# Optimization experiments

Measured on AMD Instinct MI355X. Metric: run time of the kernel, lower is better.

Reference implementation:

```python
import jax, jax.numpy as jnp
import numpy as np

ALPHA = 0.2

def setup_inputs() -> dict:
    key = jax.random.key(0)
    k1, k2, k3, k4, k5 = jax.random.split(key, 5)
    B, N, Fin, Fout = 4, 4096, 128, 128
    x = jax.random.normal(k1, (B, N, Fin), dtype=jnp.float32)
    adj = jax.random.randint(k2, (N, N), 0, 2, dtype=jnp.int32)
    W = jax.random.normal(k3, (Fin, Fout), dtype=jnp.float32) * (1.0 / np.sqrt(Fin))
    a_src = jax.random.normal(k4, (Fout, 1), dtype=jnp.float32) * (1.0 / np.sqrt(Fout))
    a_dst = jax.random.normal(k5, (Fout, 1), dtype=jnp.float32) * (1.0 / np.sqrt(Fout))
    return {"x": x, "adj": adj, "W": W, "a_src": a_src, "a_dst": a_dst}

def reference(x, adj, W, a_src, a_dst):
    # h: (B, N, Fout)
    h = jnp.einsum('bnf,fo->bno', x, W)
    e_src = h @ a_src              # (B, N, 1)
    e_dst = h @ a_dst              # (B, N, 1)
    # additive attention scores: (B, N, N)
    e = e_src + jnp.swapaxes(e_dst, 1, 2)
    e = jnp.where(e >= 0, e, ALPHA * e)  # leaky_relu
    mask = (adj == 0)[None, :, :]
    e = jnp.where(mask, -jnp.inf, e)
    attn = jax.nn.softmax(e, axis=-1)
    attn = jnp.where(jnp.isnan(attn), 0.0, attn)  # nan_to_num for all-masked rows
    out = jnp.einsum('bij,bjo->bio', attn, h)
    return (out, attn)
```

## Files before the change

kernel.cpp:

```cpp
#include <hip/hip_runtime.h>
#include <hip/hip_bf16.h>
#include <hip/hip_fp16.h>

#define B_ 4
#define N_ 4096
#define F_ 128
#define NEG (-1e30f)

typedef _Float16 f16;
typedef _Float16 half8 __attribute__((ext_vector_type(8)));
typedef _Float16 half4 __attribute__((ext_vector_type(4)));
typedef float f32x4 __attribute__((ext_vector_type(4)));

__global__ void k_wa(const float* __restrict__ W, const float* __restrict__ a_src,
                     const float* __restrict__ a_dst, float* __restrict__ Wa) {
    int f = threadIdx.x;
    float s0 = 0.f, s1 = 0.f;
    for (int o = 0; o < F_; ++o) {
        float w = W[f * F_ + o];
        s0 += w * a_src[o];
        s1 += w * a_dst[o];
    }
    Wa[f] = s0;
    Wa[F_ + f] = s1;
}

__global__ __launch_bounds__(256) void k_h(const float* __restrict__ x,
                                           const float* __restrict__ W,
                                           f16* __restrict__ hT) {
    __shared__ float xs[16][128];
    int t = threadIdx.x;
    long R0 = (long)blockIdx.x * 16;
    const float4* xg = (const float4*)(x + R0 * 128);
    float4* xsv = (float4*)&xs[0][0];
    xsv[t] = xg[t];
    xsv[t + 256] = xg[t + 256];
    __syncthreads();
    int c = t & 127;
    int rg = t >> 7;
    float acc[8] = {0, 0, 0, 0, 0, 0, 0, 0};
    for (int k = 0; k < 128; ++k) {
        float wv = W[k * 128 + c];
        #pragma unroll
        for (int q = 0; q < 8; ++q) acc[q] += xs[rg * 8 + q][k] * wv;
    }
    int b = (int)(R0 >> 12);
    int i = (int)(R0 & 4095);
    half8 hv;
    #pragma unroll
    for (int q = 0; q < 8; ++q) hv[q] = (f16)acc[q];
    *(half8*)(hT + ((long)(b * 128 + c) * 4096 + i + rg * 8)) = hv;
}

__global__ __launch_bounds__(256) void k_e(const float* __restrict__ x,
                                           const float* __restrict__ Wa,
                                           float* __restrict__ e_src,
                                           float* __restrict__ e_dst) {
    int t = threadIdx.x;
    int lane = t & 63;
    int w = t >> 6;
    long rg = (long)blockIdx.x * 4 + w;
    const float* xr = x + rg * 128;
    float x0 = xr[lane], x1 = xr[lane + 64];
    float s = x0 * Wa[lane] + x1 * Wa[lane + 64];
    float d = x0 * Wa[128 + lane] + x1 * Wa[192 + lane];
    #pragma unroll
    for (int off = 32; off; off >>= 1) {
        s += __shfl_xor(s, off, 64);
        d += __shfl_xor(d, off, 64);
    }
    if (lane == 0) { e_src[rg] = s; e_dst[rg] = d; }
}

__global__ __launch_bounds__(256) void k_attn(const int* __restrict__ adj,
                                              const float* __restrict__ e_src,
                                              const float* __restrict__ e_dst,
                                              float* __restrict__ attn) {
    int rg = blockIdx.x;
    int b = rg >> 12;
    int i = rg & 4095;
    int t = threadIdx.x;
    float es = e_src[rg];
    const int* arow = adj + (long)i * N_;
    const float* ed = e_dst + b * N_;
    float p[16];
    float m = NEG;
    #pragma unroll
    for (int c = 0; c < 16; ++c) {
        int j = t + 256 * c;
        int a = arow[j];
        float e = es + ed[j];
        e = (e >= 0.f) ? e : 0.2f * e;
        e = a ? e : NEG;
        p[c] = e;
        m = fmaxf(m, e);
    }
    #pragma unroll
    for (int off = 32; off; off >>= 1) m = fmaxf(m, __shfl_xor(m, off, 64));
    __shared__ float sred[8];
    int lane = t & 63, wid = t >> 6;
    if (lane == 0) sred[wid] = m;
    __syncthreads();
    m = fmaxf(fmaxf(sred[0], sred[1]), fmaxf(sred[2], sred[3]));
    float sum = 0.f;
    #pragma unroll
    for (int c = 0; c < 16; ++c) {
        float pv = __expf(p[c] - m);
        p[c] = pv;
        sum += pv;
    }
    #pragma unroll
    for (int off = 32; off; off >>= 1) sum += __shfl_xor(sum, off, 64);
    if (lane == 0) sred[4 + wid] = sum;
    __syncthreads();
    sum = sred[4] + sred[5] + sred[6] + sred[7];
    float inv = (m <= -1e29f) ? 0.f : 1.f / sum;
    float* orow = attn + (long)rg * N_;
    #pragma unroll
    for (int c = 0; c < 16; ++c) orow[t + 256 * c] = p[c] * inv;
}

__global__ __launch_bounds__(256) void k_out(const float* __restrict__ attn,
                                             const f16* __restrict__ hT,
                                             float* __restrict__ out) {
    __shared__ __align__(16) f16 Alds[32][40];
    __shared__ __align__(16) f16 Blds[128][40];
    int t = threadIdx.x;
    int bx = blockIdx.x;
    int b = bx >> 7;
    int i0 = (bx & 127) * 32;
    const float* Ab = attn + ((long)b * N_ + i0) * N_;
    const f16* Bb = hT + (long)b * 128 * 4096;

    int lane = t & 63, wid = t >> 6;
    int strip = (wid & 1) * 16;
    int cb = (wid >> 1) * 64;
    int r16 = lane & 15;
    int kq = (lane >> 4) * 8;

    f32x4 acc[4] = {{0,0,0,0}, {0,0,0,0}, {0,0,0,0}, {0,0,0,0}};

    int ar = t >> 3;
    int akc = (t & 7) * 4;
    int bc = t & 127;
    int bh = t >> 7;

    for (int kt = 0; kt < 128; ++kt) {
        int k0 = kt * 32;
        __syncthreads();
        float4 av = *(const float4*)(Ab + (long)ar * N_ + k0 + akc);
        half4 a4;
        a4[0] = (f16)av.x; a4[1] = (f16)av.y; a4[2] = (f16)av.z; a4[3] = (f16)av.w;
        *(half4*)&Alds[ar][akc] = a4;
        const f16* bsrc = Bb + (long)bc * 4096 + k0 + bh * 16;
        half8 b0 = *(const half8*)(bsrc);
        half8 b1 = *(const half8*)(bsrc + 8);
        *(half8*)&Blds[bc][bh * 16] = b0;
        *(half8*)&Blds[bc][bh * 16 + 8] = b1;
        __syncthreads();
        half8 af = *(const half8*)&Alds[strip + r16][kq];
        #pragma unroll
        for (int nt = 0; nt < 4; ++nt) {
            half8 bf = *(const half8*)&Blds[cb + nt * 16 + r16][kq];
            acc[nt] = __builtin_amdgcn_mfma_f32_16x16x32_f16(af, bf, acc[nt], 0, 0, 0);
        }
    }
    int rbase = i0 + strip + (lane >> 4) * 4;
    float* ob = out + (long)b * N_ * 128;
    #pragma unroll
    for (int nt = 0; nt < 4; ++nt) {
        int col = cb + nt * 16 + r16;
        #pragma unroll
        for (int reg = 0; reg < 4; ++reg) {
            ob[(long)(rbase + reg) * 128 + col] = acc[nt][reg];
        }
    }
}

extern "C" void kernel_launch(void* const* d_in, const int* in_sizes, int n_in,
                              void* d_out, int out_size, void* d_ws, size_t ws_size,
                              hipStream_t stream) {
    const float* x     = (const float*)d_in[0];
    const int*   adj   = (const int*)d_in[1];
    const float* W     = (const float*)d_in[2];
    const float* a_src = (const float*)d_in[3];
    const float* a_dst = (const float*)d_in[4];
    float* out  = (float*)d_out;
    float* attn = out + (long)B_ * N_ * F_;

    char* ws = (char*)d_ws;
    float* Wa    = (float*)(ws + 0);
    float* e_src = (float*)(ws + 1024);
    float* e_dst = (float*)(ws + 66560);
    f16*   hT    = (f16*)(ws + 132096);

    k_wa<<<dim3(1), dim3(128), 0, stream>>>(W, a_src, a_dst, Wa);
    k_h<<<dim3((B_ * N_) / 16), dim3(256), 0, stream>>>(x, W, hT);
    k_e<<<dim3((B_ * N_) / 4), dim3(256), 0, stream>>>(x, Wa, e_src, e_dst);
    k_attn<<<dim3(B_ * N_), dim3(256), 0, stream>>>(adj, e_src, e_dst, attn);
    k_out<<<dim3(B_ * (N_ / 32)), dim3(256), 0, stream>>>(attn, hT, out);
}
```

Measured before the change: 525.5 us.

## Load MFMA fragments directly from global with register double-buffering in k_out

```diff
diff --git a/kernel.cpp b/kernel.cpp
--- a/kernel.cpp
+++ b/kernel.cpp
@@ -9,7 +9,6 @@
 
 typedef _Float16 f16;
 typedef _Float16 half8 __attribute__((ext_vector_type(8)));
-typedef _Float16 half4 __attribute__((ext_vector_type(4)));
 typedef float f32x4 __attribute__((ext_vector_type(4)));
 
 __global__ void k_wa(const float* __restrict__ W, const float* __restrict__ a_src,
@@ -123,56 +122,84 @@
 __global__ __launch_bounds__(256) void k_out(const float* __restrict__ attn,
                                              const f16* __restrict__ hT,
                                              float* __restrict__ out) {
-    __shared__ __align__(16) f16 Alds[32][40];
-    __shared__ __align__(16) f16 Blds[128][40];
-    int t = threadIdx.x;
+    int t = threadIdx.x;
+    int lane = t & 63, wid = t >> 6;
     int bx = blockIdx.x;
     int b = bx >> 7;
     int i0 = (bx & 127) * 32;
-    const float* Ab = attn + ((long)b * N_ + i0) * N_;
-    const f16* Bb = hT + (long)b * 128 * 4096;
-
-    int lane = t & 63, wid = t >> 6;
+    int r16 = lane & 15;
+    int kq = (lane >> 4) * 8;
     int strip = (wid & 1) * 16;
     int cb = (wid >> 1) * 64;
-    int r16 = lane & 15;
-    int kq = (lane >> 4) * 8;
-
-    f32x4 acc[4] = {{0,0,0,0}, {0,0,0,0}, {0,0,0,0}, {0,0,0,0}};
-
-    int ar = t >> 3;
-    int akc = (t & 7) * 4;
-    int bc = t & 127;
-    int bh = t >> 7;
-
-    for (int kt = 0; kt < 128; ++kt) {
-        int k0 = kt * 32;
-        __syncthreads();
-        float4 av = *(const float4*)(Ab + (long)ar * N_ + k0 + akc);
-        half4 a4;
-        a4[0] = (f16)av.x; a4[1] = (f16)av.y; a4[2] = (f16)av.z; a4[3] = (f16)av.w;
-        *(half4*)&Alds[ar][akc] = a4;
-        const f16* bsrc = Bb + (long)bc * 4096 + k0 + bh * 16;
-        half8 b0 = *(const half8*)(bsrc);
-        half8 b1 = *(const half8*)(bsrc + 8);
-        *(half8*)&Blds[bc][bh * 16] = b0;
-        *(half8*)&Blds[bc][bh * 16 + 8] = b1;
-        __syncthreads();
-        half8 af = *(const half8*)&Alds[strip + r16][kq];
-        #pragma unroll
-        for (int nt = 0; nt < 4; ++nt) {
-            half8 bf = *(const half8*)&Blds[cb + nt * 16 + r16][kq];
-            acc[nt] = __builtin_amdgcn_mfma_f32_16x16x32_f16(af, bf, acc[nt], 0, 0, 0);
-        }
-    }
+
+    const float* Ap = attn + ((long)b * N_ + i0 + strip + r16) * N_ + kq;
+    const f16* Bp = hT + ((long)(b * F_ + cb + r16)) * (long)N_ + kq;
+
+    f32x4 acc[4] = {{0,0,0,0},{0,0,0,0},{0,0,0,0},{0,0,0,0}};
+
+    f32x4 cA[2][2], nA[2][2];
+    half8 cB[2][4], nB[2][4];
+
+    #pragma unroll
+    for (int s = 0; s < 2; ++s) {
+        cA[s][0] = *(const f32x4*)(Ap + s * 32);
+        cA[s][1] = *(const f32x4*)(Ap + s * 32 + 4);
+        #pragma unroll
+        for (int nt = 0; nt < 4; ++nt)
+            cB[s][nt] = *(const half8*)(Bp + (long)nt * (16 * N_) + s * 32);
+    }
+
+    for (int kt = 1; kt < 64; ++kt) {
+        int k0 = kt * 64;
+        #pragma unroll
+        for (int s = 0; s < 2; ++s) {
+            nA[s][0] = *(const f32x4*)(Ap + k0 + s * 32);
+            nA[s][1] = *(const f32x4*)(Ap + k0 + s * 32 + 4);
+            #pragma unroll
+            for (int nt = 0; nt < 4; ++nt)
+                nB[s][nt] = *(const half8*)(Bp + (long)nt * (16 * N_) + k0 + s * 32);
+        }
+        #pragma unroll
+        for (int s = 0; s < 2; ++s) {
+            half8 af;
+            #pragma unroll
+            for (int q = 0; q < 4; ++q) {
+                af[q] = (f16)cA[s][0][q];
+                af[q + 4] = (f16)cA[s][1][q];
+            }
+            #pragma unroll
+            for (int nt = 0; nt < 4; ++nt)
+                acc[nt] = __builtin_amdgcn_mfma_f32_16x16x32_f16(af, cB[s][nt], acc[nt], 0, 0, 0);
+        }
+        #pragma unroll
+        for (int s = 0; s < 2; ++s) {
+            cA[s][0] = nA[s][0];
+            cA[s][1] = nA[s][1];
+            #pragma unroll
+            for (int nt = 0; nt < 4; ++nt) cB[s][nt] = nB[s][nt];
+        }
+    }
+    #pragma unroll
+    for (int s = 0; s < 2; ++s) {
+        half8 af;
+        #pragma unroll
+        for (int q = 0; q < 4; ++q) {
+            af[q] = (f16)cA[s][0][q];
+            af[q + 4] = (f16)cA[s][1][q];
+        }
+        #pragma unroll
+        for (int nt = 0; nt < 4; ++nt)
+            acc[nt] = __builtin_amdgcn_mfma_f32_16x16x32_f16(af, cB[s][nt], acc[nt], 0, 0, 0);
+    }
+
     int rbase = i0 + strip + (lane >> 4) * 4;
-    float* ob = out + (long)b * N_ * 128;
+    float* ob = out + (long)b * N_ * F_;
     #pragma unroll
     for (int nt = 0; nt < 4; ++nt) {
         int col = cb + nt * 16 + r16;
         #pragma unroll
         for (int reg = 0; reg < 4; ++reg) {
-            ob[(long)(rbase + reg) * 128 + col] = acc[nt][reg];
+            ob[(long)(rbase + reg) * F_ + col] = acc[nt][reg];
         }
     }
 }
```

Measured after the change: 546.3 us. 1.04x slower.

## Fuse attention weight recomputation with attn@h matmul using precomputed row stats

Applied to the files above, without the earlier changes.

```diff
diff --git a/kernel.cpp b/kernel.cpp
--- a/kernel.cpp
+++ b/kernel.cpp
@@ -9,17 +9,20 @@
 
 typedef _Float16 f16;
 typedef _Float16 half8 __attribute__((ext_vector_type(8)));
-typedef _Float16 half4 __attribute__((ext_vector_type(4)));
 typedef float f32x4 __attribute__((ext_vector_type(4)));
 
 __global__ void k_wa(const float* __restrict__ W, const float* __restrict__ a_src,
                      const float* __restrict__ a_dst, float* __restrict__ Wa) {
     int f = threadIdx.x;
+    const float4* Wr = (const float4*)(W + f * F_);
+    const float4* As = (const float4*)a_src;
+    const float4* Ad = (const float4*)a_dst;
     float s0 = 0.f, s1 = 0.f;
-    for (int o = 0; o < F_; ++o) {
-        float w = W[f * F_ + o];
-        s0 += w * a_src[o];
-        s1 += w * a_dst[o];
+    #pragma unroll
+    for (int o = 0; o < 32; ++o) {
+        float4 w = Wr[o], s = As[o], d = Ad[o];
+        s0 += w.x * s.x + w.y * s.y + w.z * s.z + w.w * s.w;
+        s1 += w.x * d.x + w.y * d.y + w.z * d.z + w.w * d.w;
     }
     Wa[f] = s0;
     Wa[F_ + f] = s1;
@@ -39,6 +42,7 @@
     int c = t & 127;
     int rg = t >> 7;
     float acc[8] = {0, 0, 0, 0, 0, 0, 0, 0};
+    #pragma unroll 4
     for (int k = 0; k < 128; ++k) {
         float wv = W[k * 128 + c];
         #pragma unroll
@@ -72,17 +76,19 @@
     if (lane == 0) { e_src[rg] = s; e_dst[rg] = d; }
 }
 
-__global__ __launch_bounds__(256) void k_attn(const int* __restrict__ adj,
-                                              const float* __restrict__ e_src,
-                                              const float* __restrict__ e_dst,
-                                              float* __restrict__ attn) {
-    int rg = blockIdx.x;
-    int b = rg >> 12;
-    int i = rg & 4095;
+__global__ __launch_bounds__(256) void k_stats(const int* __restrict__ adj,
+                                               const float* __restrict__ e_src,
+                                               const float* __restrict__ e_dst,
+                                               float* __restrict__ stat_m,
+                                               float* __restrict__ stat_inv) {
+    int bx = blockIdx.x;
+    int b = bx & 3;
+    int i = bx >> 2;
+    long rg = (long)b * N_ + i;
     int t = threadIdx.x;
     float es = e_src[rg];
     const int* arow = adj + (long)i * N_;
-    const float* ed = e_dst + b * N_;
+    const float* ed = e_dst + (long)b * N_;
     float p[16];
     float m = NEG;
     #pragma unroll
@@ -104,76 +110,107 @@
     m = fmaxf(fmaxf(sred[0], sred[1]), fmaxf(sred[2], sred[3]));
     float sum = 0.f;
     #pragma unroll
-    for (int c = 0; c < 16; ++c) {
-        float pv = __expf(p[c] - m);
-        p[c] = pv;
-        sum += pv;
-    }
+    for (int c = 0; c < 16; ++c) sum += __expf(p[c] - m);
     #pragma unroll
     for (int off = 32; off; off >>= 1) sum += __shfl_xor(sum, off, 64);
     if (lane == 0) sred[4 + wid] = sum;
     __syncthreads();
-    sum = sred[4] + sred[5] + sred[6] + sred[7];
-    float inv = (m <= -1e29f) ? 0.f : 1.f / sum;
-    float* orow = attn + (long)rg * N_;
-    #pragma unroll
-    for (int c = 0; c < 16; ++c) orow[t + 256 * c] = p[c] * inv;
-}
-
-__global__ __launch_bounds__(256) void k_out(const float* __restrict__ attn,
-                                             const f16* __restrict__ hT,
-                                             float* __restrict__ out) {
-    __shared__ __align__(16) f16 Alds[32][40];
-    __shared__ __align__(16) f16 Blds[128][40];
-    int t = threadIdx.x;
+    if (t == 0) {
+        sum = sred[4] + sred[5] + sred[6] + sred[7];
+        float inv = (m <= -1e29f) ? 0.f : 1.f / sum;
+        stat_m[rg] = m;
+        stat_inv[rg] = inv;
+    }
+}
+
+__device__ __forceinline__ void tile_step(
+    const int* Aj, const float* Ed, const f16* Bp, float* Ao,
+    int j0, int jn, float es, float m, float inv, int q4,
+    int4& a0c, int4& a1c, float4& e0c, float4& e1c,
+    int4& a0n, int4& a1n, float4& e0n, float4& e1n,
+    f32x4& acc0, f32x4& acc1) {
+    a0n = *(const int4*)(Aj + jn);
+    a1n = *(const int4*)(Aj + jn + 4);
+    e0n = *(const float4*)(Ed + jn);
+    e1n = *(const float4*)(Ed + jn + 4);
+    half8 bf0 = *(const half8*)(Bp + j0);
+    half8 bf1 = *(const half8*)(Bp + j0 + 16 * N_);
+    int am[8] = {a0c.x, a0c.y, a0c.z, a0c.w, a1c.x, a1c.y, a1c.z, a1c.w};
+    float ev[8] = {e0c.x, e0c.y, e0c.z, e0c.w, e1c.x, e1c.y, e1c.z, e1c.w};
+    float pv[8];
+    #pragma unroll
+    for (int q = 0; q < 8; ++q) {
+        float e = es + ev[q];
+        e = (e >= 0.f) ? e : 0.2f * e;
+        e = am[q] ? e : NEG;
+        pv[q] = __expf(e - m);
+    }
+    if (q4 == 0) {
+        f32x4 w0 = {pv[0] * inv, pv[1] * inv, pv[2] * inv, pv[3] * inv};
+        f32x4 w1 = {pv[4] * inv, pv[5] * inv, pv[6] * inv, pv[7] * inv};
+        __builtin_nontemporal_store(w0, (f32x4*)(Ao + j0));
+        __builtin_nontemporal_store(w1, (f32x4*)(Ao + j0 + 4));
+    }
+    half8 af;
+    #pragma unroll
+    for (int q = 0; q < 8; ++q) af[q] = (f16)pv[q];
+    acc0 = __builtin_amdgcn_mfma_f32_16x16x32_f16(af, bf0, acc0, 0, 0, 0);
+    acc1 = __builtin_amdgcn_mfma_f32_16x16x32_f16(af, bf1, acc1, 0, 0, 0);
+}
+
+__global__ __launch_bounds__(256) void k_fused(const int* __restrict__ adj,
+                                               const float* __restrict__ e_src,
+                                               const float* __restrict__ e_dst,
+                                               const float* __restrict__ stat_m,
+                                               const float* __restrict__ stat_inv,
+                                               const f16* __restrict__ hT,
+                                               float* __restrict__ attn,
+                                               float* __restrict__ out) {
+    int t = threadIdx.x;
+    int lane = t & 63, wid = t >> 6;
     int bx = blockIdx.x;
-    int b = bx >> 7;
-    int i0 = (bx & 127) * 32;
-    const float* Ab = attn + ((long)b * N_ + i0) * N_;
-    const f16* Bb = hT + (long)b * 128 * 4096;
-
-    int lane = t & 63, wid = t >> 6;
-    int strip = (wid & 1) * 16;
-    int cb = (wid >> 1) * 64;
+    int b = bx >> 8;
+    int i0 = (bx & 255) * 16;
     int r16 = lane & 15;
     int kq = (lane >> 4) * 8;
-
-    f32x4 acc[4] = {{0,0,0,0}, {0,0,0,0}, {0,0,0,0}, {0,0,0,0}};
-
-    int ar = t >> 3;
-    int akc = (t & 7) * 4;
-    int bc = t & 127;
-    int bh = t >> 7;
-
-    for (int kt = 0; kt < 128; ++kt) {
-        int k0 = kt * 32;
-        __syncthreads();
-        float4 av = *(const float4*)(Ab + (long)ar * N_ + k0 + akc);
-        half4 a4;
-        a4[0] = (f16)av.x; a4[1] = (f16)av.y; a4[2] = (f16)av.z; a4[3] = (f16)av.w;
-        *(half4*)&Alds[ar][akc] = a4;
-        const f16* bsrc = Bb + (long)bc * 4096 + k0 + bh * 16;
-        half8 b0 = *(const half8*)(bsrc);
-        half8 b1 = *(const half8*)(bsrc + 8);
-        *(half8*)&Blds[bc][bh * 16] = b0;
-        *(half8*)&Blds[bc][bh * 16 + 8] = b1;
-        __syncthreads();
-        half8 af = *(const half8*)&Alds[strip + r16][kq];
-        #pragma unroll
-        for (int nt = 0; nt < 4; ++nt) {
-            half8 bf = *(const half8*)&Blds[cb + nt * 16 + r16][kq];
-            acc[nt] = __builtin_amdgcn_mfma_f32_16x16x32_f16(af, bf, acc[nt], 0, 0, 0);
-        }
-    }
-    int rbase = i0 + strip + (lane >> 4) * 4;
-    float* ob = out + (long)b * N_ * 128;
-    #pragma unroll
-    for (int nt = 0; nt < 4; ++nt) {
-        int col = cb + nt * 16 + r16;
-        #pragma unroll
-        for (int reg = 0; reg < 4; ++reg) {
-            ob[(long)(rbase + reg) * 128 + col] = acc[nt][reg];
-        }
+    int q4 = wid;
+    int row = i0 + r16;
+    long rg = (long)b * N_ + row;
+    float es = e_src[rg];
+    float m = stat_m[rg];
+    float inv = stat_inv[rg];
+    const int* Aj = adj + (long)row * N_ + kq;
+    const float* Ed = e_dst + (long)b * N_ + kq;
+    float* Ao = attn + rg * (long)N_ + kq;
+    const f16* Bp = hT + ((long)(b * F_ + q4 * 32 + r16)) * N_ + kq;
+
+    f32x4 acc0 = {0, 0, 0, 0}, acc1 = {0, 0, 0, 0};
+
+    int4 a0A, a1A, a0B, a1B;
+    float4 e0A, e1A, e0B, e1B;
+    a0A = *(const int4*)(Aj);
+    a1A = *(const int4*)(Aj + 4);
+    e0A = *(const float4*)(Ed);
+    e1A = *(const float4*)(Ed + 4);
+
+    for (int jt = 0; jt < 128; jt += 2) {
+        int j0 = jt * 32;
+        int jn2 = (jt + 2 < 128) ? (j0 + 64) : 0;
+        tile_step(Aj, Ed, Bp, Ao, j0, j0 + 32, es, m, inv, q4,
+                  a0A, a1A, e0A, e1A, a0B, a1B, e0B, e1B, acc0, acc1);
+        tile_step(Aj, Ed, Bp, Ao, j0 + 32, jn2, es, m, inv, q4,
+                  a0B, a1B, e0B, e1B, a0A, a1A, e0A, e1A, acc0, acc1);
+    }
+
+    float4 inv4 = *(const float4*)(stat_inv + (long)b * N_ + i0 + (lane >> 4) * 4);
+    float invr[4] = {inv4.x, inv4.y, inv4.z, inv4.w};
+    int rbase = i0 + (lane >> 4) * 4;
+    float* ob = out + (long)b * N_ * F_;
+    int col0 = q4 * 32 + r16;
+    #pragma unroll
+    for (int reg = 0; reg < 4; ++reg) {
+        ob[(long)(rbase + reg) * F_ + col0]      = acc0[reg] * invr[reg];
+        ob[(long)(rbase + reg) * F_ + col0 + 16] = acc1[reg] * invr[reg];
     }
 }
 
@@ -189,14 +226,17 @@
     float* attn = out + (long)B_ * N_ * F_;
 
     char* ws = (char*)d_ws;
-    float* Wa    = (float*)(ws + 0);
-    float* e_src = (float*)(ws + 1024);
-    float* e_dst = (float*)(ws + 66560);
-    f16*   hT    = (f16*)(ws + 132096);
+    float* Wa       = (float*)(ws + 0);
+    float* e_src    = (float*)(ws + 1024);
+    float* e_dst    = (float*)(ws + 66560);
+    f16*   hT       = (f16*)(ws + 132096);
+    float* stat_m   = (float*)(ws + 4326400);
+    float* stat_inv = (float*)(ws + 4391936);
 
     k_wa<<<dim3(1), dim3(128), 0, stream>>>(W, a_src, a_dst, Wa);
+    k_e<<<dim3((B_ * N_) / 4), dim3(256), 0, stream>>>(x, Wa, e_src, e_dst);
     k_h<<<dim3((B_ * N_) / 16), dim3(256), 0, stream>>>(x, W, hT);
-    k_e<<<dim3((B_ * N_) / 4), dim3(256), 0, stream>>>(x, Wa, e_src, e_dst);
-    k_attn<<<dim3(B_ * N_), dim3(256), 0, stream>>>(adj, e_src, e_dst, attn);
-    k_out<<<dim3(B_ * (N_ / 32)), dim3(256), 0, stream>>>(attn, hT, out);
-}
+    k_stats<<<dim3(B_ * N_), dim3(256), 0, stream>>>(adj, e_src, e_dst, stat_m, stat_inv);
+    k_fused<<<dim3(B_ * (N_ / 16)), dim3(256), 0, stream>>>(adj, e_src, e_dst, stat_m,
+                                                            stat_inv, hT, attn, out);
+}
```

Result: slower. 609.6 us (+16.0%).
